# Kernel tuning notes

Measured on AMD Instinct MI355X. Metric: run time of the kernel, lower is better.

Reference implementation:

```python
import jax, jax.numpy as jnp
import numpy as np

K = 7          # kernel_size
PAD = 3        # padding (same-size output)
GROUPS = 8


def _unfold(z, H, W):
    # z: [B, C, H+2p, W+2p] -> patches [B, C, H, W, K*K], flat index = kh*K + kw
    # matches torch .unfold(2,K,1).unfold(3,K,1).view(..., -1)
    return jnp.stack(
        [z[:, :, a:a + H, b:b + W] for a in range(K) for b in range(K)],
        axis=-1,
    )


def setup_inputs() -> dict:
    key = jax.random.key(0)
    ks = jax.random.split(key, 7)
    B, C, H, W = 4, 64, 64, 64
    Cout = 64
    fan_scale = (2.0 / Cout) ** 0.5  # kaiming fan_out, 1x1 conv
    return {
        "x": jax.random.normal(ks[0], (B, C, H, W), jnp.float32),
        "y": jax.random.normal(ks[1], (B, C, H, W), jnp.float32),
        "Wq": jax.random.normal(ks[2], (Cout, C), jnp.float32) * fan_scale,
        "Wk": jax.random.normal(ks[3], (Cout, C), jnp.float32) * fan_scale,
        "Wv": jax.random.normal(ks[4], (Cout, C), jnp.float32) * fan_scale,
        "rel_h": jax.random.normal(ks[5], (Cout // 2, K), jnp.float32),
        "rel_w": jax.random.normal(ks[6], (Cout // 2, K), jnp.float32),
    }


def reference(x, y, Wq, Wk, Wv, rel_h, rel_w):
    B, C, H, W = x.shape
    Cout = Wq.shape[0]
    half = Cout // 2

    # 1x1 convs (no bias) commute with zero padding, so project first.
    q = jnp.einsum('oc,bchw->bohw', Wq, x)          # [B, Cout, H, W]
    k_full = jnp.einsum('oc,bchw->bohw', Wk, x)
    v_full = jnp.einsum('oc,bchw->bohw', Wv, y)

    pad4 = ((0, 0), (0, 0), (PAD, PAD), (PAD, PAD))
    k_pat = _unfold(jnp.pad(k_full, pad4), H, W)    # [B, Cout, H, W, K*K]
    v_pat = _unfold(jnp.pad(v_full, pad4), H, W)

    # relative-position bias: rel_h over kh (top half of channels), rel_w over kw
    bias_h = jnp.broadcast_to(rel_h[:, :, None], (half, K, K))   # [Cout/2, kh, kw]
    bias_w = jnp.broadcast_to(rel_w[:, None, :], (half, K, K))
    bias = jnp.concatenate([bias_h, bias_w], axis=0).reshape(Cout, K * K)
    k_pat = k_pat + bias[None, :, None, None, :]

    cg = Cout // GROUPS
    k_pat = k_pat.reshape(B, GROUPS, cg, H, W, K * K)
    v_pat = v_pat.reshape(B, GROUPS, cg, H, W, K * K)
    q = q.reshape(B, GROUPS, cg, H, W, 1)

    attn = jax.nn.softmax(q * k_pat, axis=-1)       # per-channel softmax over window
    out = jnp.sum(attn * v_pat, axis=-1)            # [B, G, cg, H, W]
    return out.reshape(B, Cout, H, W)
```

## Files before the change

kernel.cpp:

```cpp
#include <hip/hip_runtime.h>

#define HW 4096

typedef float f4 __attribute__((ext_vector_type(4)));

__global__ __launch_bounds__(256) void proj_kernel(
    const float* __restrict__ x, const float* __restrict__ y,
    const float* __restrict__ Wq, const float* __restrict__ Wk,
    const float* __restrict__ Wv,
    float* __restrict__ q, float* __restrict__ k, float* __restrict__ v)
{
    __shared__ float wlds[64 * 24];
    const int t = threadIdx.x;
    const int g = blockIdx.y;

#pragma unroll
    for (int m = 0; m < 3; ++m) {
        const float* W = (m == 0) ? Wq : (m == 1) ? Wk : Wv;
#pragma unroll
        for (int hh = 0; hh < 2; ++hh) {
            const int r = hh * 256 + t;
            const int i = r >> 6, c = r & 63;
            wlds[c * 24 + m * 8 + i] = W[g * 512 + r];
        }
    }
    __syncthreads();

    const int px  = blockIdx.x * 256 + t;
    const int b   = px >> 12;
    const int pib = px & 4095;
    const float* xb = x + (size_t)b * 64 * HW + pib;
    const float* yb = y + (size_t)b * 64 * HW + pib;

    float aq[8], ak[8], av[8];
#pragma unroll
    for (int i = 0; i < 8; ++i) { aq[i] = 0.f; ak[i] = 0.f; av[i] = 0.f; }

#pragma unroll 16
    for (int c = 0; c < 64; ++c) {
        const float xv = xb[c * HW];
        const float yv = yb[c * HW];
        const f4 wq0 = *(const f4*)&wlds[c * 24 + 0];
        const f4 wq1 = *(const f4*)&wlds[c * 24 + 4];
        const f4 wk0 = *(const f4*)&wlds[c * 24 + 8];
        const f4 wk1 = *(const f4*)&wlds[c * 24 + 12];
        const f4 wv0 = *(const f4*)&wlds[c * 24 + 16];
        const f4 wv1 = *(const f4*)&wlds[c * 24 + 20];
#pragma unroll
        for (int i = 0; i < 4; ++i) {
            aq[i]     = fmaf(wq0[i], xv, aq[i]);
            aq[i + 4] = fmaf(wq1[i], xv, aq[i + 4]);
            ak[i]     = fmaf(wk0[i], xv, ak[i]);
            ak[i + 4] = fmaf(wk1[i], xv, ak[i + 4]);
            av[i]     = fmaf(wv0[i], yv, av[i]);
            av[i + 4] = fmaf(wv1[i], yv, av[i + 4]);
        }
    }

#pragma unroll
    for (int i = 0; i < 8; ++i) {
        const size_t o = ((size_t)b * 64 + g * 8 + i) * HW + pib;
        q[o] = aq[i];
        k[o] = ak[i];
        v[o] = av[i];
    }
}

template<bool BIAS_H>
__device__ __forceinline__ void attn_body(
    const float* kT, const float* vT, int r, int w0,
    const float qe[4], const float qb[7][4], float l[4], float o[4])
{
#pragma unroll
    for (int a = 0; a < 7; ++a) {
        const float* kr = &kT[(r + a) * 72 + w0];
        const float* vr = &vT[(r + a) * 72 + w0];
        const f4 k0 = *(const f4*)(kr), k1 = *(const f4*)(kr + 4), k2 = *(const f4*)(kr + 8);
        const f4 v0 = *(const f4*)(vr), v1 = *(const f4*)(vr + 4), v2 = *(const f4*)(vr + 8);
        const float kw[12] = {k0[0], k0[1], k0[2], k0[3], k1[0], k1[1], k1[2], k1[3],
                              k2[0], k2[1], k2[2], k2[3]};
        const float vw[12] = {v0[0], v0[1], v0[2], v0[3], v1[0], v1[1], v1[2], v1[3],
                              v2[0], v2[1], v2[2], v2[3]};
#pragma unroll
        for (int b2 = 0; b2 < 7; ++b2) {
#pragma unroll
            for (int p = 0; p < 4; ++p) {
                float s = fmaf(qe[p], kw[p + b2 + 1], qb[BIAS_H ? a : b2][p]);
                s = fminf(s, 115.0f);
                const float e = __builtin_amdgcn_exp2f(s);
                l[p] += e;
                o[p] = fmaf(e, vw[p + b2 + 1], o[p]);
            }
        }
    }
}

__global__ __launch_bounds__(256) void attn_kernel(
    const float* __restrict__ qg, const float* __restrict__ kg,
    const float* __restrict__ vg,
    const float* __restrict__ rel_h, const float* __restrict__ rel_w,
    float* __restrict__ out)
{
    __shared__ float kT[22 * 72];
    __shared__ float vT[22 * 72];

    const int blk = blockIdx.x;
    const int bc  = blk >> 2;
    const int h0  = (blk & 3) << 4;
    const int c   = bc & 63;
    const int t   = threadIdx.x;

    const float* kimg = kg + (size_t)bc * HW;
    const float* vimg = vg + (size_t)bc * HW;
    const f4 z4 = {0.f, 0.f, 0.f, 0.f};

    if (t < 88) {
        const int row = t >> 2, side = (t >> 1) & 1, arr = t & 1;
        float* dst = arr ? vT : kT;
        *(f4*)&dst[row * 72 + side * 68] = z4;
    }
#pragma unroll
    for (int j = 0; j < 2; ++j) {
        const int idx = j * 256 + t;
        if (idx < 352) {
            const int row = idx >> 4, ch = idx & 15;
            const int hy = h0 - 3 + row;
            const bool rv = ((unsigned)hy < 64u);
            const f4 kv = rv ? *(const f4*)&kimg[hy * 64 + ch * 4] : z4;
            const f4 vv = rv ? *(const f4*)&vimg[hy * 64 + ch * 4] : z4;
            *(f4*)&kT[row * 72 + ch * 4 + 4] = kv;
            *(f4*)&vT[row * 72 + ch * 4 + 4] = vv;
        }
    }
    __syncthreads();

    const int r  = t >> 4;
    const int w0 = (t & 15) << 2;
    const int h  = h0 + r;

    const float LOG2E = 1.4426950408889634f;
    const f4 qv = *(const f4*)&qg[(size_t)bc * HW + h * 64 + w0];
    float qe[4];
#pragma unroll
    for (int p = 0; p < 4; ++p) qe[p] = qv[p] * LOG2E;

    float qb[7][4];
    if (c < 32) {
#pragma unroll
        for (int a = 0; a < 7; ++a) {
            const float bh = rel_h[c * 7 + a];
#pragma unroll
            for (int p = 0; p < 4; ++p) qb[a][p] = qe[p] * bh;
        }
    } else {
#pragma unroll
        for (int j = 0; j < 7; ++j) {
            const float bw = rel_w[(c - 32) * 7 + j];
#pragma unroll
            for (int p = 0; p < 4; ++p) qb[j][p] = qe[p] * bw;
        }
    }

    float l[4] = {0.f, 0.f, 0.f, 0.f};
    float o[4] = {0.f, 0.f, 0.f, 0.f};
    if (c < 32) attn_body<true >(kT, vT, r, w0, qe, qb, l, o);
    else        attn_body<false>(kT, vT, r, w0, qe, qb, l, o);

    f4 res;
#pragma unroll
    for (int p = 0; p < 4; ++p)
        res[p] = o[p] * __builtin_amdgcn_rcpf(l[p]);
    *(f4*)&out[(size_t)bc * HW + h * 64 + w0] = res;
}

extern "C" void kernel_launch(void* const* d_in, const int* in_sizes, int n_in,
                              void* d_out, int out_size, void* d_ws, size_t ws_size,
                              hipStream_t stream) {
    const float* x   = (const float*)d_in[0];
    const float* y   = (const float*)d_in[1];
    const float* Wq  = (const float*)d_in[2];
    const float* Wk  = (const float*)d_in[3];
    const float* Wv  = (const float*)d_in[4];
    const float* rlh = (const float*)d_in[5];
    const float* rlw = (const float*)d_in[6];
    float* out = (float*)d_out;

    float* q = (float*)d_ws;
    float* k = q + (1 << 20);
    float* v = k + (1 << 20);

    dim3 gA(64, 8);
    proj_kernel<<<gA, 256, 0, stream>>>(x, y, Wq, Wk, Wv, q, k, v);
    attn_kernel<<<1024, 256, 0, stream>>>(q, k, v, rlh, rlw, out);
}
```

Measured before the change: 109.9 us.

## Retile projection kernel for full weight reuse and unify attention bias path

The projection kernel now stages all three 64x64 weight matrices in LDS. Each thread computes 2 output channels by 8 pixels for q, k and v using vector x/y loads, which cuts redundant re-reading of x and y across the 8 group blocks; the grid shrinks from 512 to 256 blocks. The attention kernel drops the templated h/w bias bodies in favour of a single loop that adds a combined bias to k before multiplying by q. That saves registers for the precomputed q*bias table but adds an extra add per window element. The larger LDS footprint and fewer blocks may lower occupancy in the projection step.

```diff
diff --git a/kernel.cpp b/kernel.cpp
--- a/kernel.cpp
+++ b/kernel.cpp
@@ -3,6 +3,9 @@
 #define HW 4096
 
 typedef float f4 __attribute__((ext_vector_type(4)));
+typedef float f2 __attribute__((ext_vector_type(2)));
+
+#define WSTRIDE 194
 
 __global__ __launch_bounds__(256) void proj_kernel(
     const float* __restrict__ x, const float* __restrict__ y,
@@ -10,88 +13,71 @@
     const float* __restrict__ Wv,
     float* __restrict__ q, float* __restrict__ k, float* __restrict__ v)
 {
-    __shared__ float wlds[64 * 24];
+    __shared__ float wlds[64 * WSTRIDE];
     const int t = threadIdx.x;
-    const int g = blockIdx.y;
 
+    {
+        const float* Ws[3] = {Wq, Wk, Wv};
 #pragma unroll
-    for (int m = 0; m < 3; ++m) {
-        const float* W = (m == 0) ? Wq : (m == 1) ? Wk : Wv;
+        for (int m = 0; m < 3; ++m) {
 #pragma unroll
-        for (int hh = 0; hh < 2; ++hh) {
-            const int r = hh * 256 + t;
-            const int i = r >> 6, c = r & 63;
-            wlds[c * 24 + m * 8 + i] = W[g * 512 + r];
+            for (int s = 0; s < 4; ++s) {
+                const int fi = s * 256 + t;
+                const int co = fi >> 4, c4 = fi & 15;
+                const f4 w = *(const f4*)&Ws[m][co * 64 + c4 * 4];
+#pragma unroll
+                for (int i = 0; i < 4; ++i)
+                    wlds[(c4 * 4 + i) * WSTRIDE + m * 64 + co] = w[i];
+            }
         }
     }
     __syncthreads();
 
-    const int px  = blockIdx.x * 256 + t;
-    const int b   = px >> 12;
-    const int pib = px & 4095;
-    const float* xb = x + (size_t)b * 64 * HW + pib;
-    const float* yb = y + (size_t)b * 64 * HW + pib;
+    const int cg  = t & 31;
+    const int pq  = t >> 5;
+    const int px0 = blockIdx.x * 64;
+    const int b   = px0 >> 12;
+    const int poff = (px0 & 4095) + pq * 8;
+    const float* xb = x + (size_t)b * 64 * HW + poff;
+    const float* yb = y + (size_t)b * 64 * HW + poff;
 
-    float aq[8], ak[8], av[8];
+    f4 acc[3][2][2];
 #pragma unroll
-    for (int i = 0; i < 8; ++i) { aq[i] = 0.f; ak[i] = 0.f; av[i] = 0.f; }
+    for (int m = 0; m < 3; ++m)
+#pragma unroll
+        for (int i = 0; i < 2; ++i)
+#pragma unroll
+            for (int h = 0; h < 2; ++h)
+                acc[m][i][h] = (f4){0.f, 0.f, 0.f, 0.f};
 
-#pragma unroll 16
+#pragma unroll 4
     for (int c = 0; c < 64; ++c) {
-        const float xv = xb[c * HW];
-        const float yv = yb[c * HW];
-        const f4 wq0 = *(const f4*)&wlds[c * 24 + 0];
-        const f4 wq1 = *(const f4*)&wlds[c * 24 + 4];
-        const f4 wk0 = *(const f4*)&wlds[c * 24 + 8];
-        const f4 wk1 = *(const f4*)&wlds[c * 24 + 12];
-        const f4 wv0 = *(const f4*)&wlds[c * 24 + 16];
-        const f4 wv1 = *(const f4*)&wlds[c * 24 + 20];
-#pragma unroll
-        for (int i = 0; i < 4; ++i) {
-            aq[i]     = fmaf(wq0[i], xv, aq[i]);
-            aq[i + 4] = fmaf(wq1[i], xv, aq[i + 4]);
-            ak[i]     = fmaf(wk0[i], xv, ak[i]);
-            ak[i + 4] = fmaf(wk1[i], xv, ak[i + 4]);
-            av[i]     = fmaf(wv0[i], yv, av[i]);
-            av[i + 4] = fmaf(wv1[i], yv, av[i + 4]);
-        }
+        const f4 xv0 = *(const f4*)&xb[c * HW];
+        const f4 xv1 = *(const f4*)&xb[c * HW + 4];
+        const f4 yv0 = *(const f4*)&yb[c * HW];
+        const f4 yv1 = *(const f4*)&yb[c * HW + 4];
+        const float* wr = &wlds[c * WSTRIDE + 2 * cg];
+        const f2 wq = *(const f2*)&wr[0];
+        const f2 wk = *(const f2*)&wr[64];
+        const f2 wv = *(const f2*)&wr[128];
+        acc[0][0][0] += xv0 * wq[0];  acc[0][0][1] += xv1 * wq[0];
+        acc[0][1][0] += xv0 * wq[1];  acc[0][1][1] += xv1 * wq[1];
+        acc[1][0][0] += xv0 * wk[0];  acc[1][0][1] += xv1 * wk[0];
+        acc[1][1][0] += xv0 * wk[1];  acc[1][1][1] += xv1 * wk[1];
+        acc[2][0][0] += yv0 * wv[0];  acc[2][0][1] += yv1 * wv[0];
+        acc[2][1][0] += yv0 * wv[1];  acc[2][1][1] += yv1 * wv[1];
     }
 
+    {
+        float* outs[3] = {q, k, v};
 #pragma unroll
-    for (int i = 0; i < 8; ++i) {
-        const size_t o = ((size_t)b * 64 + g * 8 + i) * HW + pib;
-        q[o] = aq[i];
-        k[o] = ak[i];
-        v[o] = av[i];
-    }
-}
-
-template<bool BIAS_H>
-__device__ __forceinline__ void attn_body(
-    const float* kT, const float* vT, int r, int w0,
-    const float qe[4], const float qb[7][4], float l[4], float o[4])
-{
+        for (int m = 0; m < 3; ++m)
 #pragma unroll
-    for (int a = 0; a < 7; ++a) {
-        const float* kr = &kT[(r + a) * 72 + w0];
-        const float* vr = &vT[(r + a) * 72 + w0];
-        const f4 k0 = *(const f4*)(kr), k1 = *(const f4*)(kr + 4), k2 = *(const f4*)(kr + 8);
-        const f4 v0 = *(const f4*)(vr), v1 = *(const f4*)(vr + 4), v2 = *(const f4*)(vr + 8);
-        const float kw[12] = {k0[0], k0[1], k0[2], k0[3], k1[0], k1[1], k1[2], k1[3],
-                              k2[0], k2[1], k2[2], k2[3]};
-        const float vw[12] = {v0[0], v0[1], v0[2], v0[3], v1[0], v1[1], v1[2], v1[3],
-                              v2[0], v2[1], v2[2], v2[3]};
-#pragma unroll
-        for (int b2 = 0; b2 < 7; ++b2) {
-#pragma unroll
-            for (int p = 0; p < 4; ++p) {
-                float s = fmaf(qe[p], kw[p + b2 + 1], qb[BIAS_H ? a : b2][p]);
-                s = fminf(s, 115.0f);
-                const float e = __builtin_amdgcn_exp2f(s);
-                l[p] += e;
-                o[p] = fmaf(e, vw[p + b2 + 1], o[p]);
+            for (int i = 0; i < 2; ++i) {
+                float* dst = outs[m] + ((size_t)b * 64 + 2 * cg + i) * HW + poff;
+                *(f4*)&dst[0] = acc[m][i][0];
+                *(f4*)&dst[4] = acc[m][i][1];
             }
-        }
     }
 }
 
@@ -144,27 +130,45 @@
 #pragma unroll
     for (int p = 0; p < 4; ++p) qe[p] = qv[p] * LOG2E;
 
-    float qb[7][4];
+    float bh[7], bw[7];
     if (c < 32) {
 #pragma unroll
-        for (int a = 0; a < 7; ++a) {
-            const float bh = rel_h[c * 7 + a];
-#pragma unroll
-            for (int p = 0; p < 4; ++p) qb[a][p] = qe[p] * bh;
-        }
+        for (int a = 0; a < 7; ++a) { bh[a] = rel_h[c * 7 + a]; bw[a] = 0.f; }
     } else {
 #pragma unroll
-        for (int j = 0; j < 7; ++j) {
-            const float bw = rel_w[(c - 32) * 7 + j];
-#pragma unroll
-            for (int p = 0; p < 4; ++p) qb[j][p] = qe[p] * bw;
-        }
+        for (int a = 0; a < 7; ++a) { bh[a] = 0.f; bw[a] = rel_w[(c - 32) * 7 + a]; }
     }
 
     float l[4] = {0.f, 0.f, 0.f, 0.f};
     float o[4] = {0.f, 0.f, 0.f, 0.f};
-    if (c < 32) attn_body<true >(kT, vT, r, w0, qe, qb, l, o);
-    else        attn_body<false>(kT, vT, r, w0, qe, qb, l, o);
+
+#pragma unroll
+    for (int a = 0; a < 7; ++a) {
+        const int ro = (r + a) * 72 + w0;
+        const f4 k0 = *(const f4*)&kT[ro];
+        const f4 k1 = *(const f4*)&kT[ro + 4];
+        const f4 k2 = *(const f4*)&kT[ro + 8];
+        const f4 v0 = *(const f4*)&vT[ro];
+        const f4 v1 = *(const f4*)&vT[ro + 4];
+        const f4 v2 = *(const f4*)&vT[ro + 8];
+        const float kw[12] = {k0[0], k0[1], k0[2], k0[3], k1[0], k1[1], k1[2], k1[3],
+                              k2[0], k2[1], k2[2], k2[3]};
+        const float vw[12] = {v0[0], v0[1], v0[2], v0[3], v1[0], v1[1], v1[2], v1[3],
+                              v2[0], v2[1], v2[2], v2[3]};
+        const float bha = bh[a];
+#pragma unroll
+        for (int b2 = 0; b2 < 7; ++b2) {
+            const float bias = bha + bw[b2];
+#pragma unroll
+            for (int p = 0; p < 4; ++p) {
+                float s = qe[p] * (kw[p + b2 + 1] + bias);
+                s = fminf(s, 115.f);
+                const float e = __builtin_amdgcn_exp2f(s);
+                l[p] += e;
+                o[p] = fmaf(e, vw[p + b2 + 1], o[p]);
+            }
+        }
+    }
 
     f4 res;
 #pragma unroll
@@ -189,7 +193,6 @@
     float* k = q + (1 << 20);
     float* v = k + (1 << 20);
 
-    dim3 gA(64, 8);
-    proj_kernel<<<gA, 256, 0, stream>>>(x, y, Wq, Wk, Wv, q, k, v);
+    proj_kernel<<<256, 256, 0, stream>>>(x, y, Wq, Wk, Wv, q, k, v);
     attn_kernel<<<1024, 256, 0, stream>>>(q, k, v, rlh, rlw, out);
 }
```

Measured after the change: 97.68 us. 1.12x faster.
